# Kernel optimization log

Hardware: AMD Instinct MI355X
Metric: run time of the kernel (lower is better)

## Reference

```python
import jax, jax.numpy as jnp
import numpy as np

N_AXIS = 128      # n_x_axis == n_y_axis
N_TARGET = 8192


def setup_inputs() -> dict:
    key = jax.random.key(0)
    k1, k2 = jax.random.split(key, 2)
    # decoder output feature map: (4, n_y, n_x)
    feature_map = jax.random.normal(k1, (4, N_AXIS, N_AXIS), dtype=jnp.float32)
    # encoder grid: regular 2d grid in [-3, 3]^2, flattened (n_x*n_y, 2)
    ax = jnp.linspace(-3.0, 3.0, N_AXIS, dtype=jnp.float32)
    gx, gy = jnp.meshgrid(ax, ax, indexing='ij')
    grid = jnp.stack([gx, gy], axis=-1).reshape(N_AXIS * N_AXIS, 2)
    # target points in the same domain
    X_target = jax.random.uniform(k2, (N_TARGET, 2), dtype=jnp.float32,
                                  minval=-3.0, maxval=3.0)
    l_scale = jnp.float32(1.0)
    return {"feature_map": feature_map, "grid": grid,
            "X_target": X_target, "l_scale": l_scale}


def reference(feature_map, grid, X_target, l_scale):
    n_y, n_x = feature_map.shape[1], feature_map.shape[2]
    # Means_grid = FM[:2].permute(2,1,0).reshape(n_x*n_y, 2)
    means_grid = jnp.transpose(feature_map[:2], (2, 1, 0)).reshape(n_x * n_y, 2)
    # Sigmas_grid = softplus(FM[2:]), same permute/reshape
    sigmas_grid = jnp.transpose(jax.nn.softplus(feature_map[2:]), (2, 1, 0)).reshape(n_x * n_y, 2)
    # RBF kernel between targets and grid: K[t,g] = exp(-||xt-xg||^2 / (2 l^2))
    d2 = jnp.sum((X_target[:, None, :] - grid[None, :, :]) ** 2, axis=-1)  # [T, G]
    K = jnp.exp(-0.5 * d2 / (l_scale ** 2))
    denom = jnp.sum(K, axis=1, keepdims=True)  # normalized (Nadaraya-Watson)
    means_target = (K @ means_grid) / denom    # [T, 2]
    sigmas_target = (K @ sigmas_grid) / denom  # [T, 2]
    return means_target, sigmas_target
```

## Files before the change

kernel.cpp:

```cpp
#include <hip/hip_runtime.h>
#include <hip/hip_bf16.h>
#include <math.h>


#define NA      128
#define TT      16
#define TILES   2
#define THREADS 512

typedef __attribute__((ext_vector_type(8))) short short8;
typedef __attribute__((ext_vector_type(4))) float f32x4;

__device__ __forceinline__ short f2bf(float x) {
    __hip_bfloat16 h = __float2bfloat16(x);
    return *reinterpret_cast<short*>(&h);
}

__global__ __launch_bounds__(128)
void pack_pre(const float* __restrict__ fm, short* __restrict__ bfB)
{
    const int idx = blockIdx.x * 128 + threadIdx.x;
    const int c  = idx >> 12;
    const int k  = (idx >> 5) & 127;
    const int i0 = (idx & 31) * 4;

    float4 v = *reinterpret_cast<const float4*>(fm + c * NA * NA + k * NA + i0);
    if (c >= 2) {
        v.x = (v.x > 15.0f) ? v.x : log1pf(__expf(v.x));
        v.y = (v.y > 15.0f) ? v.y : log1pf(__expf(v.y));
        v.z = (v.z > 15.0f) ? v.z : log1pf(__expf(v.z));
        v.w = (v.w > 15.0f) ? v.w : log1pf(__expf(v.w));
    }
    const int s  = k >> 5;
    const int e  = k & 7;
    const int Lk = ((k >> 3) & 3) * 16;
    const float vv[4] = {v.x, v.y, v.z, v.w};
#pragma unroll
    for (int d = 0; d < 4; ++d) {
        const int i = i0 + d;
        const int n = i >> 4;
        const int L = Lk + (i & 15);
        bfB[(((c * 8 + n) * 4 + s) * 64 + L) * 8 + e] = f2bf(vv[d]);
    }
}

__global__ __launch_bounds__(THREADS)
void cnp_mfma(const short* __restrict__ bfB,
              const float* __restrict__ grid,
              const float* __restrict__ xt,
              const float* __restrict__ lsp,
              float* __restrict__ out,
              int n_target)
{
    __shared__ __attribute__((aligned(16))) float Kx[TT * NA];
    __shared__ __attribute__((aligned(16))) float Ky32[TT * NA];
    __shared__ __attribute__((aligned(16))) short kyA[4 * 64 * 8];
    __shared__ float psx[TT], psy[TT];
    __shared__ float red[4][2][TT];

    const int tid   = threadIdx.x;
    const int wid   = tid >> 6;
    const int c     = wid & 3;
    const int nh    = wid >> 2;
    const int lane  = tid & 63;
    const int tbase = blockIdx.x * (TT * TILES);

    const short8* bbase = reinterpret_cast<const short8*>(bfB)
                        + c * 2048 + nh * 1024 + lane;
    const short8 b00 = bbase[0],         b01 = bbase[64],
                 b02 = bbase[128],       b03 = bbase[192];
    const short8 b10 = bbase[256],       b11 = bbase[256 + 64],
                 b12 = bbase[256 + 128], b13 = bbase[256 + 192];
    const short8 b20 = bbase[512],       b21 = bbase[512 + 64],
                 b22 = bbase[512 + 128], b23 = bbase[512 + 192];
    const short8 b30 = bbase[768],       b31 = bbase[768 + 64],
                 b32 = bbase[768 + 128], b33 = bbase[768 + 192];

    const float l      = lsp[0];
    const float inv2l2 = 0.5f / (l * l);

    const int icol = lane & 15;
    const int tb   = (lane >> 4) * 4;

    for (int tt = 0; tt < TILES; ++tt) {
        const int t0 = tbase + tt * TT;

#pragma unroll
        for (int s = 0; s < 4; ++s) {
            const int k = s * THREADS + tid;
            const int t = k >> 7;
            const int j = k & 127;
            int tg = t0 + t; if (tg >= n_target) tg = n_target - 1;
            const float ax = grid[j * 2 + 1];
            const float dx = xt[tg * 2 + 0] - ax;
            const float dy = xt[tg * 2 + 1] - ax;
            const float kxv = __expf(-dx * dx * inv2l2);
            const float kyv = __expf(-dy * dy * inv2l2);
            Kx[t * NA + j]   = kxv;
            Ky32[t * NA + j] = kyv;
            const int ss = j >> 5, g = (j & 31) >> 3, e = j & 7;
            kyA[((ss * 64) + g * 16 + (t & 15)) * 8 + e] = f2bf(kyv);
        }
        __syncthreads();

        {
            const int grp  = tid >> 4;
            const int l16  = tid & 15;
            const int t    = grp >> 1;
            const int axis = grp & 1;
            const float* kb = axis ? Ky32 : Kx;
            const float4 q0 = *reinterpret_cast<const float4*>(&kb[t * NA + l16 * 8]);
            const float4 q1 = *reinterpret_cast<const float4*>(&kb[t * NA + l16 * 8 + 4]);
            float u = ((q0.x + q0.y) + (q0.z + q0.w)) + ((q1.x + q1.y) + (q1.z + q1.w));
            u += __shfl_xor(u, 1); u += __shfl_xor(u, 2);
            u += __shfl_xor(u, 4); u += __shfl_xor(u, 8);
            if (l16 == 0) { if (axis) psy[t] = u; else psx[t] = u; }
        }

        const short8* kap = reinterpret_cast<const short8*>(kyA);
        const short8 a0 = kap[0 * 64 + lane];
        const short8 a1 = kap[1 * 64 + lane];
        const short8 a2 = kap[2 * 64 + lane];
        const short8 a3 = kap[3 * 64 + lane];

        f32x4 p = {0.f, 0.f, 0.f, 0.f};
#define NTILE(NN, B0, B1, B2, B3)                                              \
        {                                                                      \
            f32x4 acc = {0.f, 0.f, 0.f, 0.f};                                  \
            acc = __builtin_amdgcn_mfma_f32_16x16x32_bf16(a0, B0, acc, 0, 0, 0); \
            acc = __builtin_amdgcn_mfma_f32_16x16x32_bf16(a1, B1, acc, 0, 0, 0); \
            acc = __builtin_amdgcn_mfma_f32_16x16x32_bf16(a2, B2, acc, 0, 0, 0); \
            acc = __builtin_amdgcn_mfma_f32_16x16x32_bf16(a3, B3, acc, 0, 0, 0); \
            const int i = (nh * 4 + (NN)) * 16 + icol;                         \
            p.x = fmaf(Kx[(tb + 0) * NA + i], acc.x, p.x);                     \
            p.y = fmaf(Kx[(tb + 1) * NA + i], acc.y, p.y);                     \
            p.z = fmaf(Kx[(tb + 2) * NA + i], acc.z, p.z);                     \
            p.w = fmaf(Kx[(tb + 3) * NA + i], acc.w, p.w);                     \
        }
        NTILE(0, b00, b01, b02, b03)
        NTILE(1, b10, b11, b12, b13)
        NTILE(2, b20, b21, b22, b23)
        NTILE(3, b30, b31, b32, b33)
#undef NTILE

#pragma unroll
        for (int st = 1; st <= 8; st <<= 1) {
            p.x += __shfl_xor(p.x, st);
            p.y += __shfl_xor(p.y, st);
            p.z += __shfl_xor(p.z, st);
            p.w += __shfl_xor(p.w, st);
        }
        if (icol == 0) {
            red[c][nh][tb + 0] = p.x;
            red[c][nh][tb + 1] = p.y;
            red[c][nh][tb + 2] = p.z;
            red[c][nh][tb + 3] = p.w;
        }
        __syncthreads();

        if (tid < 4 * TT) {
            const int t  = tid & (TT - 1);
            const int cc = tid >> 4;
            const int tg = t0 + t;
            if (tg < n_target) {
                const float numer = red[cc][0][t] + red[cc][1][t];
                const float val = numer / (psx[t] * psy[t]);
                if (cc < 2) out[tg * 2 + cc] = val;
                else        out[n_target * 2 + tg * 2 + (cc - 2)] = val;
            }
        }
    }
}

extern "C" void kernel_launch(void* const* d_in, const int* in_sizes, int n_in,
                              void* d_out, int out_size, void* d_ws, size_t ws_size,
                              hipStream_t stream) {
    const float* fm   = (const float*)d_in[0];
    const float* grid = (const float*)d_in[1];
    const float* xt   = (const float*)d_in[2];
    const float* lsp  = (const float*)d_in[3];
    float* out = (float*)d_out;
    short* bfB = (short*)d_ws;

    const int n_target = in_sizes[2] / 2;

    hipLaunchKernelGGL(pack_pre, dim3(128), dim3(128), 0, stream, fm, bfB);

    const int blocks = (n_target + TT * TILES - 1) / (TT * TILES);
    hipLaunchKernelGGL(cnp_mfma, dim3(blocks), dim3(THREADS), 0, stream,
                       bfB, grid, xt, lsp, out, n_target);
}
```

Baseline: 15.41 us.

## Fuse feature-map packing and softplus into the main MFMA kernel

Removes the separate pack_pre launch. Each block of the main kernel now stages the full 4x128x128 feature map through shared memory in four XOR-swizzled chunks, applies softplus to the sigma channels, and builds its bf16 B fragments in registers. This saves a kernel launch and the workspace round trip. In exchange, all 256 blocks redundantly read the 256KB feature map and recompute softplus, and shared memory use grows by 64KB per block, which may limit occupancy.

```diff
diff --git a/kernel.cpp b/kernel.cpp
--- a/kernel.cpp
+++ b/kernel.cpp
@@ -16,42 +16,15 @@
     return *reinterpret_cast<short*>(&h);
 }
 
-__global__ __launch_bounds__(128)
-void pack_pre(const float* __restrict__ fm, short* __restrict__ bfB)
+__global__ __launch_bounds__(THREADS)
+void cnp_one(const float* __restrict__ fm,
+             const float* __restrict__ grid,
+             const float* __restrict__ xt,
+             const float* __restrict__ lsp,
+             float* __restrict__ out,
+             int n_target)
 {
-    const int idx = blockIdx.x * 128 + threadIdx.x;
-    const int c  = idx >> 12;
-    const int k  = (idx >> 5) & 127;
-    const int i0 = (idx & 31) * 4;
-
-    float4 v = *reinterpret_cast<const float4*>(fm + c * NA * NA + k * NA + i0);
-    if (c >= 2) {
-        v.x = (v.x > 15.0f) ? v.x : log1pf(__expf(v.x));
-        v.y = (v.y > 15.0f) ? v.y : log1pf(__expf(v.y));
-        v.z = (v.z > 15.0f) ? v.z : log1pf(__expf(v.z));
-        v.w = (v.w > 15.0f) ? v.w : log1pf(__expf(v.w));
-    }
-    const int s  = k >> 5;
-    const int e  = k & 7;
-    const int Lk = ((k >> 3) & 3) * 16;
-    const float vv[4] = {v.x, v.y, v.z, v.w};
-#pragma unroll
-    for (int d = 0; d < 4; ++d) {
-        const int i = i0 + d;
-        const int n = i >> 4;
-        const int L = Lk + (i & 15);
-        bfB[(((c * 8 + n) * 4 + s) * 64 + L) * 8 + e] = f2bf(vv[d]);
-    }
-}
-
-__global__ __launch_bounds__(THREADS)
-void cnp_mfma(const short* __restrict__ bfB,
-              const float* __restrict__ grid,
-              const float* __restrict__ xt,
-              const float* __restrict__ lsp,
-              float* __restrict__ out,
-              int n_target)
-{
+    __shared__ __attribute__((aligned(16))) float fmS[4 * 32 * NA];
     __shared__ __attribute__((aligned(16))) float Kx[TT * NA];
     __shared__ __attribute__((aligned(16))) float Ky32[TT * NA];
     __shared__ __attribute__((aligned(16))) short kyA[4 * 64 * 8];
@@ -63,24 +36,61 @@
     const int c     = wid & 3;
     const int nh    = wid >> 2;
     const int lane  = tid & 63;
+    const int g     = lane >> 4;
+    const int m     = lane & 15;
     const int tbase = blockIdx.x * (TT * TILES);
-
-    const short8* bbase = reinterpret_cast<const short8*>(bfB)
-                        + c * 2048 + nh * 1024 + lane;
-    const short8 b00 = bbase[0],         b01 = bbase[64],
-                 b02 = bbase[128],       b03 = bbase[192];
-    const short8 b10 = bbase[256],       b11 = bbase[256 + 64],
-                 b12 = bbase[256 + 128], b13 = bbase[256 + 192];
-    const short8 b20 = bbase[512],       b21 = bbase[512 + 64],
-                 b22 = bbase[512 + 128], b23 = bbase[512 + 192];
-    const short8 b30 = bbase[768],       b31 = bbase[768 + 64],
-                 b32 = bbase[768 + 128], b33 = bbase[768 + 192];
 
     const float l      = lsp[0];
     const float inv2l2 = 0.5f / (l * l);
 
-    const int icol = lane & 15;
-    const int tb   = (lane >> 4) * 4;
+    short8 b00, b01, b02, b03, b10, b11, b12, b13;
+    short8 b20, b21, b22, b23, b30, b31, b32, b33;
+
+#define SP1(z) z = ((z) > 15.0f) ? (z) : log1pf(__expf(z))
+#define STAGE(S)                                                               \
+    _Pragma("unroll")                                                          \
+    for (int q = 0; q < 8; ++q) {                                              \
+        const int f4  = q * 512 + tid;                                         \
+        const int cc  = f4 >> 10;                \
+        const int rem = f4 & 1023;                                             \
+        const int kk  = rem >> 5;                                              \
+        const int i4  = (rem & 31) << 2;                                       \
+        float4 v = *reinterpret_cast<const float4*>(                           \
+            fm + cc * (NA * NA) + ((S) * 32 + kk) * NA + i4);                  \
+        if (q >= 4) { SP1(v.x); SP1(v.y); SP1(v.z); SP1(v.w); }                \
+        *reinterpret_cast<float4*>(                                            \
+            &fmS[(cc * 32 + kk) * NA + (i4 ^ ((kk >> 3) << 3))]) = v;          \
+    }
+
+#define FRAG(BN, NN)                                                           \
+    {                                                                          \
+        const int ibase = (((nh * 4 + (NN)) * 16 + m) ^ (g << 3));             \
+        const float* rp = &fmS[(c * 32 + g * 8) * NA + ibase];                 \
+        short8 bv;                                                             \
+        bv[0] = f2bf(rp[0 * NA]); bv[1] = f2bf(rp[1 * NA]);                    \
+        bv[2] = f2bf(rp[2 * NA]); bv[3] = f2bf(rp[3 * NA]);                    \
+        bv[4] = f2bf(rp[4 * NA]); bv[5] = f2bf(rp[5 * NA]);                    \
+        bv[6] = f2bf(rp[6 * NA]); bv[7] = f2bf(rp[7 * NA]);                    \
+        BN = bv;                                                               \
+    }
+
+#define CHUNK(S, BA, BB, BC, BD)                                               \
+    STAGE(S)                                                                   \
+    __syncthreads();                                                           \
+    FRAG(BA, 0) FRAG(BB, 1) FRAG(BC, 2) FRAG(BD, 3)                            \
+    __syncthreads();
+
+    CHUNK(0, b00, b10, b20, b30)
+    CHUNK(1, b01, b11, b21, b31)
+    CHUNK(2, b02, b12, b22, b32)
+    CHUNK(3, b03, b13, b23, b33)
+#undef CHUNK
+#undef FRAG
+#undef STAGE
+#undef SP1
+
+    const int icol = m;
+    const int tb   = g * 4;
 
     for (int tt = 0; tt < TILES; ++tt) {
         const int t0 = tbase + tt * TT;
@@ -98,8 +108,8 @@
             const float kyv = __expf(-dy * dy * inv2l2);
             Kx[t * NA + j]   = kxv;
             Ky32[t * NA + j] = kyv;
-            const int ss = j >> 5, g = (j & 31) >> 3, e = j & 7;
-            kyA[((ss * 64) + g * 16 + (t & 15)) * 8 + e] = f2bf(kyv);
+            const int ss = j >> 5, gg = (j & 31) >> 3, e = j & 7;
+            kyA[((ss * 64) + gg * 16 + (t & 15)) * 8 + e] = f2bf(kyv);
         }
         __syncthreads();
 
@@ -180,13 +190,10 @@
     const float* xt   = (const float*)d_in[2];
     const float* lsp  = (const float*)d_in[3];
     float* out = (float*)d_out;
-    short* bfB = (short*)d_ws;
 
     const int n_target = in_sizes[2] / 2;
+    const int blocks = (n_target + TT * TILES - 1) / (TT * TILES);
 
-    hipLaunchKernelGGL(pack_pre, dim3(128), dim3(128), 0, stream, fm, bfB);
-
-    const int blocks = (n_target + TT * TILES - 1) / (TT * TILES);
-    hipLaunchKernelGGL(cnp_mfma, dim3(blocks), dim3(THREADS), 0, stream,
-                       bfB, grid, xt, lsp, out, n_target);
+    hipLaunchKernelGGL(cnp_one, dim3(blocks), dim3(THREADS), 0, stream,
+                       fm, grid, xt, lsp, out, n_target);
 }
```

Measured after the change: 41.18 us. 167% more time.
